# Kernel optimization log

Measured on AMD Instinct MI355X. Metric: run time of the kernel, lower is better.

Reference implementation:

```python
import jax, jax.numpy as jnp
import numpy as np
from jax import lax

B, T, I, H, C = 64, 512, 512, 1024, 1000


def _lstm_layer(x, W_ih, W_hh, b_ih, b_hh):
    # x: [B, T, in]; W_ih: [4H, in]; W_hh: [4H, H]; biases: [4H]
    # Precompute input projections for all timesteps (one big GEMM).
    xW = jnp.einsum('bti,gi->btg', x, W_ih) + b_ih + b_hh  # [B, T, 4H]
    h0 = jnp.zeros((x.shape[0], W_hh.shape[1]), x.dtype)
    c0 = jnp.zeros_like(h0)

    def step(carry, xw_t):
        h, c = carry
        gates = xw_t + h @ W_hh.T  # [B, 4H]
        i, f, g, o = jnp.split(gates, 4, axis=-1)  # PyTorch gate order i,f,g,o
        i = jax.nn.sigmoid(i)
        f = jax.nn.sigmoid(f)
        g = jnp.tanh(g)
        o = jax.nn.sigmoid(o)
        c = f * c + i * g
        h = o * jnp.tanh(c)
        return (h, c), h

    (h_T, c_T), hs = lax.scan(step, (h0, c0), jnp.swapaxes(xW, 0, 1))
    return jnp.swapaxes(hs, 0, 1), h_T  # [B, T, H], [B, H]


def setup_inputs() -> dict:
    key = jax.random.key(0)
    ks = jax.random.split(key, 11)
    s_i = 1.0 / np.sqrt(H)
    u = lambda k, shape: jax.random.uniform(k, shape, jnp.float32, -s_i, s_i)
    return {
        'x': jax.random.normal(ks[0], (B, T, I), jnp.float32),
        'W_ih0': u(ks[1], (4 * H, I)),
        'W_hh0': u(ks[2], (4 * H, H)),
        'b_ih0': u(ks[3], (4 * H,)),
        'b_hh0': u(ks[4], (4 * H,)),
        'W_ih1': u(ks[5], (4 * H, H)),
        'W_hh1': u(ks[6], (4 * H, H)),
        'b_ih1': u(ks[7], (4 * H,)),
        'b_hh1': u(ks[8], (4 * H,)),
        'W_d': u(ks[9], (C, H)),
        'b_d': u(ks[10], (C,)),
    }


def reference(x, W_ih0, W_hh0, b_ih0, b_hh0, W_ih1, W_hh1, b_ih1, b_hh1, W_d, b_d):
    h1_seq, _ = _lstm_layer(x, W_ih0, W_hh0, b_ih0, b_hh0)
    _, h_last = _lstm_layer(h1_seq, W_ih1, W_hh1, b_ih1, b_hh1)
    return h_last @ W_d.T + b_d  # [B, num_classes]
```

## Files before the change

kernel.cpp:

```cpp
#include <hip/hip_runtime.h>

typedef short short8 __attribute__((ext_vector_type(8)));
typedef float f32x4 __attribute__((ext_vector_type(4)));
typedef float f32x16 __attribute__((ext_vector_type(16)));
typedef int i32x4 __attribute__((ext_vector_type(4)));
typedef unsigned short u16;
typedef unsigned long long u64;

#define NBLK 256
#define BDIM 512
#define BB 64
#define TT 512
#define II 512
#define HH 1024
#define NCLS 1000
#define HBUF (BB*HH)

__device__ __forceinline__ u16 f2bf(float f) {
  union { float f; unsigned u; } v; v.f = f;
  unsigned u = v.u;
  u += 0x7fffu + ((u >> 16) & 1u);
  return (u16)(u >> 16);
}

__device__ __forceinline__ short8 cvt8(f32x4 a, f32x4 b) {
  short8 v;
  v[0] = (short)f2bf(a[0]); v[1] = (short)f2bf(a[1]);
  v[2] = (short)f2bf(a[2]); v[3] = (short)f2bf(a[3]);
  v[4] = (short)f2bf(b[0]); v[5] = (short)f2bf(b[1]);
  v[6] = (short)f2bf(b[2]); v[7] = (short)f2bf(b[3]);
  return v;
}

__device__ __forceinline__ unsigned ld_rlx(const unsigned* p) {
  return __hip_atomic_load(p, __ATOMIC_RELAXED, __HIP_MEMORY_SCOPE_AGENT);
}
__device__ __forceinline__ void st_rlx(unsigned* p, unsigned v) {
  __hip_atomic_store(p, v, __ATOMIC_RELAXED, __HIP_MEMORY_SCOPE_AGENT);
}

__global__ void cvt_x(const float* __restrict__ x, u16* __restrict__ xb, int n8) {
  int i = blockIdx.x * blockDim.x + threadIdx.x;
  const int stride = gridDim.x * blockDim.x;
  for (; i < n8; i += stride) {
    f32x4 a = ((const f32x4*)x)[2 * i];
    f32x4 b = ((const f32x4*)x)[2 * i + 1];
    ((short8*)xb)[i] = cvt8(a, b);
  }
}


template<int N, int B0, int MH>
__device__ __forceinline__ void run_coh(const u16* lanep,
                                        const short8 (&breg)[MH], f32x16& acc) {
  static_assert(N % 8 == 0, "");
#pragma unroll
  for (int c = 0; c < N; c += 8) {
    i32x4 av[8];
#pragma unroll
    for (int i = 0; i < 8; ++i) {
      const u16* p = lanep + (c + i) * 16;
      asm volatile("global_load_dwordx4 %0, %1, off sc0 sc1"
                   : "=v"(av[i]) : "v"(p));
    }
    asm volatile("s_waitcnt vmcnt(0)" ::: "memory");
    __builtin_amdgcn_sched_barrier(0);
#pragma unroll
    for (int i = 0; i < 8; ++i) {
      union { i32x4 q; short8 s; } u; u.q = av[i];
      acc = __builtin_amdgcn_mfma_f32_32x32x16_bf16(u.s, breg[B0 + c + i], acc, 0, 0, 0);
    }
  }
}

template<int N, int B0, int MH>
__device__ __forceinline__ void run_pb(const u16* lanep,
                                       const short8 (&breg)[MH], f32x16& acc) {
#pragma unroll
  for (int i = 0; i < N; ++i) {
    short8 av = *(const short8*)(lanep + i * 16);
    acc = __builtin_amdgcn_mfma_f32_32x32x16_bf16(av, breg[B0 + i], acc, 0, 0, 0);
  }
}

template<int N, int B0, int MH>
__device__ __forceinline__ void run_pf(const float* lanep,
                                       const short8 (&breg)[MH], f32x16& acc) {
#pragma unroll
  for (int i = 0; i < N; ++i) {
    short8 av = cvt8(*(const f32x4*)(lanep + i * 16),
                     *(const f32x4*)(lanep + i * 16 + 4));
    acc = __builtin_amdgcn_mfma_f32_32x32x16_bf16(av, breg[B0 + i], acc, 0, 0, 0);
  }
}

template<bool XBF>
__global__ __launch_bounds__(BDIM, 2) void lstm2_fused(
    const float* __restrict__ x, const u16* __restrict__ xb,
    const float* __restrict__ Wih0, const float* __restrict__ Whh0,
    const float* __restrict__ bih0, const float* __restrict__ bhh0,
    const float* __restrict__ Wih1, const float* __restrict__ Whh1,
    const float* __restrict__ bih1, const float* __restrict__ bhh1,
    u16* __restrict__ ring,
    u16* __restrict__ h1buf,
    float* __restrict__ h1f,
    unsigned* __restrict__ bar)
{
  __shared__ u16 wlds[32 * 2048];
  __shared__ float blds[32];
  float (*g4)[64][32] = (float(*)[64][32])((char*)wlds + 98304);

  const bool isL1 = (blockIdx.x >= 128);
  const int wgl = isL1 ? (int)blockIdx.x - 128 : (int)blockIdx.x;
  const int j0 = wgl * 8;
  const int KX = isL1 ? HH : II;
  const int RL = KX + HH;
  const int ROWB = RL * 2;
  const float* Wih = isL1 ? Wih1 : Wih0;
  const float* Whh = isL1 ? Whh1 : Whh0;

  {
    const int cpr = RL / 8;
    for (int idx = threadIdx.x; idx < 32 * cpr; idx += BDIM) {
      int n = idx / cpr, cb = idx - n * cpr;
      int r = ((n >> 3) << 10) + j0 + (n & 7);
      int k = cb * 8;
      const float* src = (k < KX) ? (Wih + (size_t)r * KX + k)
                                  : (Whh + (size_t)r * HH + (k - KX));
      f32x4 a = *(const f32x4*)src;
      f32x4 b = *(const f32x4*)(src + 4);
      short8 v = cvt8(a, b);
      unsigned byte = (unsigned)(n * ROWB + k * 2) ^ ((unsigned)(n & 7) << 4);
      *(short8*)((char*)wlds + byte) = v;
    }
    if (threadIdx.x < 32) {
      int n = threadIdx.x;
      int r = ((n >> 3) << 10) + j0 + (n & 7);
      blds[n] = (isL1 ? bih1[r] : bih0[r]) + (isL1 ? bhh1[r] : bhh0[r]);
    }
  }
  __syncthreads();

  const int lane = threadIdx.x & 63;
  const int wid = threadIdx.x >> 6;
  const int mp = wid & 1, kq = wid >> 1;
  const int row_a = mp * 32 + (lane & 31);
  const int sub8 = (lane >> 5) << 3;
  const char* wch = (const char*)wlds;

  const int tb = threadIdx.x >> 3, tj = threadIdx.x & 7;

  unsigned* const arrA = bar;
  unsigned* const relA = bar + 64;
  unsigned* const arrB = bar + 256;
  unsigned* const relB = bar + 320;

  float c_state = 0.f;

  auto step_tail = [&](const f32x16& acc, u16* hout, bool wf) {
    const int col = lane & 31;
    const int rbase = mp * 32 + ((lane >> 5) << 2);
#pragma unroll
    for (int r = 0; r < 16; ++r) {
      int brow = rbase + (r & 3) + ((r >> 2) << 3);
      g4[kq][brow][col] = acc[r];
    }
    __syncthreads();
    float gv[4];
#pragma unroll
    for (int g = 0; g < 4; ++g)
      gv[g] = g4[0][tb][g * 8 + tj] + g4[1][tb][g * 8 + tj]
            + g4[2][tb][g * 8 + tj] + g4[3][tb][g * 8 + tj] + blds[g * 8 + tj];
    float gi = 1.f / (1.f + __expf(-gv[0]));
    float gf = 1.f / (1.f + __expf(-gv[1]));
    float e2 = __expf(2.f * fminf(15.f, fmaxf(-15.f, gv[2])));
    float gg = (e2 - 1.f) / (e2 + 1.f);
    float go = 1.f / (1.f + __expf(-gv[3]));
    c_state = gf * c_state + gi * gg;
    float e2c = __expf(2.f * fminf(15.f, fmaxf(-15.f, c_state)));
    float th = (e2c - 1.f) / (e2c + 1.f);
    float hval = go * th;
    unsigned hu = (unsigned)f2bf(hval);
    unsigned nbv = (unsigned)__shfl_xor((int)hu, 1);
    if ((tj & 1) == 0) {
      unsigned packed = hu | (nbv << 16);
      unsigned* dst = (unsigned*)(hout + (size_t)tb * HH + j0 + tj);
      st_rlx(dst, packed);
    }
    if (wf) h1f[(size_t)tb * HH + j0 + tj] = hval;
  };

  if (!isL1) {
    short8 breg[24];
#pragma unroll
    for (int i = 0; i < 24; ++i) {
      int k = (kq * 24 + i) * 16 + sub8;
      unsigned byte = ((unsigned)((lane & 31) * ROWB + k * 2))
                      ^ ((unsigned)(lane & 7) << 4);
      breg[i] = *(const short8*)(wch + byte);
    }
    __syncthreads();

    for (int t = 0; t < TT; ++t) {
      if (t >= 3) {
        if (threadIdx.x == 0)
          while (ld_rlx(relB) < (unsigned)(t - 2)) __builtin_amdgcn_s_sleep(2);
        __syncthreads();
      }
      f32x16 acc = {};
      const u16* hb = ring + (size_t)((t + 2) % 3) * HBUF + (size_t)row_a * HH;
      if (XBF) {
        const u16* xl = xb + (size_t)t * II + (size_t)row_a * ((size_t)TT * II)
                        + kq * 384 + sub8;
        if (kq == 0)      run_pb<24, 0>(xl, breg, acc);
        else if (kq == 1) { run_pb<8, 0>(xl, breg, acc);
                            run_coh<16, 8>(hb + 0 + sub8, breg, acc); }
        else if (kq == 2) run_coh<24, 0>(hb + 256 + sub8, breg, acc);
        else              run_coh<24, 0>(hb + 640 + sub8, breg, acc);
      } else {
        const float* xl = x + (size_t)t * II + (size_t)row_a * ((size_t)TT * II)
                          + kq * 384 + sub8;
        if (kq == 0)      run_pf<24, 0>(xl, breg, acc);
        else if (kq == 1) { run_pf<8, 0>(xl, breg, acc);
                            run_coh<16, 8>(hb + 0 + sub8, breg, acc); }
        else if (kq == 2) run_coh<24, 0>(hb + 256 + sub8, breg, acc);
        else              run_coh<24, 0>(hb + 640 + sub8, breg, acc);
      }
      step_tail(acc, ring + (size_t)(t % 3) * HBUF, false);
      __syncthreads();
      if (threadIdx.x == 0) {
        unsigned old = atomicAdd(arrA, 1u);
        if (old == (unsigned)(128 * (t + 1) - 1)) st_rlx(relA, (unsigned)(t + 1));
        else if (t < TT - 1)
          while (ld_rlx(relA) < (unsigned)(t + 1)) __builtin_amdgcn_s_sleep(2);
      }
      __syncthreads();
    }
  } else {
    short8 breg[32];
#pragma unroll
    for (int i = 0; i < 32; ++i) {
      int k = (kq * 32 + i) * 16 + sub8;
      unsigned byte = ((unsigned)((lane & 31) * ROWB + k * 2))
                      ^ ((unsigned)(lane & 7) << 4);
      breg[i] = *(const short8*)(wch + byte);
    }
    __syncthreads();

    for (int t = 0; t < TT; ++t) {
      if (threadIdx.x == 0)
        while (ld_rlx(relA) < (unsigned)(t + 1)) __builtin_amdgcn_s_sleep(2);
      __syncthreads();
      f32x16 acc = {};
      const u16* lp;
      if (kq < 2)
        lp = ring + (size_t)(t % 3) * HBUF + (size_t)row_a * HH + kq * 512 + sub8;
      else
        lp = h1buf + (size_t)((t + 1) & 1) * HBUF + (size_t)row_a * HH
             + (kq - 2) * 512 + sub8;
      run_coh<32, 0>(lp, breg, acc);
      step_tail(acc, h1buf + (size_t)(t & 1) * HBUF, t == TT - 1);
      if (t < TT - 1) {
        __syncthreads();
        if (threadIdx.x == 0) {
          unsigned old = atomicAdd(arrB, 1u);
          if (old == (unsigned)(128 * (t + 1) - 1)) st_rlx(relB, (unsigned)(t + 1));
          else
            while (ld_rlx(relB) < (unsigned)(t + 1)) __builtin_amdgcn_s_sleep(2);
        }
        __syncthreads();
      }
    }
  }
}

__global__ void dense_out(const float* __restrict__ h1, const float* __restrict__ Wd,
                          const float* __restrict__ bd, float* __restrict__ out)
{
  const int b  = threadIdx.x & 63;
  const int cl = threadIdx.x >> 6;
  const int cc = blockIdx.x * 4 + cl;
  float acc = 0.f;
  const float* hrow = h1 + (size_t)b * HH;
  const float* wrow = Wd + (size_t)cc * HH;
#pragma unroll 8
  for (int k = 0; k < HH; k += 4) {
    f32x4 hv = *(const f32x4*)(hrow + k);
    f32x4 wv = *(const f32x4*)(wrow + k);
    acc += hv[0] * wv[0] + hv[1] * wv[1] + hv[2] * wv[2] + hv[3] * wv[3];
  }
  out[(size_t)b * NCLS + cc] = acc + bd[cc];
}

extern "C" void kernel_launch(void* const* d_in, const int* in_sizes, int n_in,
                              void* d_out, int out_size, void* d_ws, size_t ws_size,
                              hipStream_t stream)
{
  (void)in_sizes; (void)n_in; (void)out_size;
  const float* x    = (const float*)d_in[0];
  const float* Wih0 = (const float*)d_in[1];
  const float* Whh0 = (const float*)d_in[2];
  const float* bih0 = (const float*)d_in[3];
  const float* bhh0 = (const float*)d_in[4];
  const float* Wih1 = (const float*)d_in[5];
  const float* Whh1 = (const float*)d_in[6];
  const float* bih1 = (const float*)d_in[7];
  const float* bhh1 = (const float*)d_in[8];
  const float* Wd   = (const float*)d_in[9];
  const float* bd   = (const float*)d_in[10];

  unsigned* bar = (unsigned*)d_ws;
  float* h1f  = (float*)((char*)d_ws + 4096);
  u16* h1buf  = (u16*)((char*)d_ws + 272 * 1024);
  u16* ring   = (u16*)((char*)d_ws + 528 * 1024);
  u16* xb     = (u16*)((char*)d_ws + (1u << 20));

  const size_t needA = (1u << 20) + (size_t)BB * TT * II * 2;
  const bool tierA = (ws_size >= needA);

  hipMemsetAsync(d_ws, 0, 912 * 1024, stream);

  if (tierA) {
    hipLaunchKernelGGL(cvt_x, dim3(2048), dim3(256), 0, stream,
                       x, xb, (int)((size_t)BB * TT * II / 8));
    hipLaunchKernelGGL((lstm2_fused<true>), dim3(NBLK), dim3(BDIM), 0, stream,
                       x, xb, Wih0, Whh0, bih0, bhh0, Wih1, Whh1, bih1, bhh1,
                       ring, h1buf, h1f, bar);
  } else {
    hipLaunchKernelGGL((lstm2_fused<false>), dim3(NBLK), dim3(BDIM), 0, stream,
                       x, xb, Wih0, Whh0, bih0, bhh0, Wih1, Whh1, bih1, bhh1,
                       ring, h1buf, h1f, bar);
  }
  hipLaunchKernelGGL(dense_out, dim3(250), dim3(256), 0, stream, h1f, Wd, bd,
                     (float*)d_out);
}
```

Measured before the change: 5.521 ms.

## Replace block-level grid barriers with per-wave dependency waits and double-buffered coherent loads

The grid-wide spin barriers, where thread 0 waits and then __syncthreads, are replaced by arrive-only counters. Each wave now spins on the specific release flag its loads depend on, so waves that only read x, or that read data from an earlier step, can start without waiting for the whole grid. The ring-reuse wait for layer 0 moves to just before the h store. Separately, run_coh now uses two register buffers with partial vmcnt waits so global loads overlap MFMA work. This adds more spinning waves polling atomics and more register pressure, and the memory-ordering reasoning becomes more delicate.

```diff
diff --git a/kernel.cpp b/kernel.cpp
--- a/kernel.cpp
+++ b/kernel.cpp
@@ -38,6 +38,9 @@
 __device__ __forceinline__ void st_rlx(unsigned* p, unsigned v) {
   __hip_atomic_store(p, v, __ATOMIC_RELAXED, __HIP_MEMORY_SCOPE_AGENT);
 }
+__device__ __forceinline__ void wave_wait_ge(const unsigned* p, unsigned tgt) {
+  while (ld_rlx(p) < tgt) __builtin_amdgcn_s_sleep(1);
+}
 
 __global__ void cvt_x(const float* __restrict__ x, u16* __restrict__ xb, int n8) {
   int i = blockIdx.x * blockDim.x + threadIdx.x;
@@ -49,27 +52,42 @@
   }
 }
 
+#define ISSUE8(arr, OFF)                                                     \
+  _Pragma("unroll") for (int i_ = 0; i_ < 8; ++i_)                           \
+    asm volatile("global_load_dwordx4 %0, %1, off sc0 sc1"                   \
+                 : "=v"(arr[i_]) : "v"(lanep + ((OFF) + i_) * 16));
+#define MFMA8(arr, OFF)                                                      \
+  _Pragma("unroll") for (int i_ = 0; i_ < 8; ++i_) {                         \
+    union { i32x4 q; short8 s; } u_; u_.q = arr[i_];                         \
+    acc = __builtin_amdgcn_mfma_f32_32x32x16_bf16(u_.s, breg[B0 + (OFF) + i_],\
+                                                  acc, 0, 0, 0); }
+#define VMWAIT0 asm volatile("s_waitcnt vmcnt(0)" ::: "memory")
+#define VMWAIT8 asm volatile("s_waitcnt vmcnt(8)" ::: "memory")
+#define SCHEDB  __builtin_amdgcn_sched_barrier(0)
 
 template<int N, int B0, int MH>
 __device__ __forceinline__ void run_coh(const u16* lanep,
                                         const short8 (&breg)[MH], f32x16& acc) {
-  static_assert(N % 8 == 0, "");
-#pragma unroll
-  for (int c = 0; c < N; c += 8) {
-    i32x4 av[8];
-#pragma unroll
-    for (int i = 0; i < 8; ++i) {
-      const u16* p = lanep + (c + i) * 16;
-      asm volatile("global_load_dwordx4 %0, %1, off sc0 sc1"
-                   : "=v"(av[i]) : "v"(p));
-    }
-    asm volatile("s_waitcnt vmcnt(0)" ::: "memory");
-    __builtin_amdgcn_sched_barrier(0);
-#pragma unroll
-    for (int i = 0; i < 8; ++i) {
-      union { i32x4 q; short8 s; } u; u.q = av[i];
-      acc = __builtin_amdgcn_mfma_f32_32x32x16_bf16(u.s, breg[B0 + c + i], acc, 0, 0, 0);
-    }
+  static_assert(N == 8 || N == 16 || N == 24 || N == 32, "");
+  i32x4 avA[8], avB[8];
+  if constexpr (N == 8) {
+    ISSUE8(avA, 0);
+    VMWAIT0; SCHEDB; MFMA8(avA, 0);
+  } else if constexpr (N == 16) {
+    ISSUE8(avA, 0); ISSUE8(avB, 8);
+    VMWAIT8; SCHEDB; MFMA8(avA, 0);
+    VMWAIT0; SCHEDB; MFMA8(avB, 8);
+  } else if constexpr (N == 24) {
+    ISSUE8(avA, 0); ISSUE8(avB, 8);
+    VMWAIT8; SCHEDB; MFMA8(avA, 0); ISSUE8(avA, 16);
+    VMWAIT8; SCHEDB; MFMA8(avB, 8);
+    VMWAIT0; SCHEDB; MFMA8(avA, 16);
+  } else {
+    ISSUE8(avA, 0); ISSUE8(avB, 8);
+    VMWAIT8; SCHEDB; MFMA8(avA, 0); ISSUE8(avA, 16);
+    VMWAIT8; SCHEDB; MFMA8(avB, 8); ISSUE8(avB, 24);
+    VMWAIT8; SCHEDB; MFMA8(avA, 16);
+    VMWAIT0; SCHEDB; MFMA8(avB, 24);
   }
 }
 
@@ -157,7 +175,8 @@
 
   float c_state = 0.f;
 
-  auto step_tail = [&](const f32x16& acc, u16* hout, bool wf) {
+  auto step_tail = [&](const f32x16& acc, u16* hout, unsigned ringtgt, bool wf,
+                       unsigned* arr, unsigned* rel, int t) {
     const int col = lane & 31;
     const int rbase = mp * 32 + ((lane >> 5) << 2);
 #pragma unroll
@@ -180,6 +199,7 @@
     float e2c = __expf(2.f * fminf(15.f, fmaxf(-15.f, c_state)));
     float th = (e2c - 1.f) / (e2c + 1.f);
     float hval = go * th;
+    if (ringtgt) wave_wait_ge(relB, ringtgt);
     unsigned hu = (unsigned)f2bf(hval);
     unsigned nbv = (unsigned)__shfl_xor((int)hu, 1);
     if ((tj & 1) == 0) {
@@ -188,6 +208,11 @@
       st_rlx(dst, packed);
     }
     if (wf) h1f[(size_t)tb * HH + j0 + tj] = hval;
+    __syncthreads();
+    if (threadIdx.x == 0) {
+      unsigned old = atomicAdd(arr, 1u);
+      if (old == (unsigned)(128 * (t + 1) - 1)) st_rlx(rel, (unsigned)(t + 1));
+    }
   };
 
   if (!isL1) {
@@ -202,11 +227,6 @@
     __syncthreads();
 
     for (int t = 0; t < TT; ++t) {
-      if (t >= 3) {
-        if (threadIdx.x == 0)
-          while (ld_rlx(relB) < (unsigned)(t - 2)) __builtin_amdgcn_s_sleep(2);
-        __syncthreads();
-      }
       f32x16 acc = {};
       const u16* hb = ring + (size_t)((t + 2) % 3) * HBUF + (size_t)row_a * HH;
       if (XBF) {
@@ -214,27 +234,26 @@
                         + kq * 384 + sub8;
         if (kq == 0)      run_pb<24, 0>(xl, breg, acc);
         else if (kq == 1) { run_pb<8, 0>(xl, breg, acc);
+                            wave_wait_ge(relA, (unsigned)t);
                             run_coh<16, 8>(hb + 0 + sub8, breg, acc); }
-        else if (kq == 2) run_coh<24, 0>(hb + 256 + sub8, breg, acc);
-        else              run_coh<24, 0>(hb + 640 + sub8, breg, acc);
+        else if (kq == 2) { wave_wait_ge(relA, (unsigned)t);
+                            run_coh<24, 0>(hb + 256 + sub8, breg, acc); }
+        else              { wave_wait_ge(relA, (unsigned)t);
+                            run_coh<24, 0>(hb + 640 + sub8, breg, acc); }
       } else {
         const float* xl = x + (size_t)t * II + (size_t)row_a * ((size_t)TT * II)
                           + kq * 384 + sub8;
         if (kq == 0)      run_pf<24, 0>(xl, breg, acc);
         else if (kq == 1) { run_pf<8, 0>(xl, breg, acc);
+                            wave_wait_ge(relA, (unsigned)t);
                             run_coh<16, 8>(hb + 0 + sub8, breg, acc); }
-        else if (kq == 2) run_coh<24, 0>(hb + 256 + sub8, breg, acc);
-        else              run_coh<24, 0>(hb + 640 + sub8, breg, acc);
+        else if (kq == 2) { wave_wait_ge(relA, (unsigned)t);
+                            run_coh<24, 0>(hb + 256 + sub8, breg, acc); }
+        else              { wave_wait_ge(relA, (unsigned)t);
+                            run_coh<24, 0>(hb + 640 + sub8, breg, acc); }
       }
-      step_tail(acc, ring + (size_t)(t % 3) * HBUF, false);
-      __syncthreads();
-      if (threadIdx.x == 0) {
-        unsigned old = atomicAdd(arrA, 1u);
-        if (old == (unsigned)(128 * (t + 1) - 1)) st_rlx(relA, (unsigned)(t + 1));
-        else if (t < TT - 1)
-          while (ld_rlx(relA) < (unsigned)(t + 1)) __builtin_amdgcn_s_sleep(2);
-      }
-      __syncthreads();
+      step_tail(acc, ring + (size_t)(t % 3) * HBUF,
+                (t >= 3) ? (unsigned)(t - 2) : 0u, false, arrA, relA, t);
     }
   } else {
     short8 breg[32];
@@ -248,28 +267,20 @@
     __syncthreads();
 
     for (int t = 0; t < TT; ++t) {
-      if (threadIdx.x == 0)
-        while (ld_rlx(relA) < (unsigned)(t + 1)) __builtin_amdgcn_s_sleep(2);
-      __syncthreads();
       f32x16 acc = {};
-      const u16* lp;
-      if (kq < 2)
-        lp = ring + (size_t)(t % 3) * HBUF + (size_t)row_a * HH + kq * 512 + sub8;
-      else
-        lp = h1buf + (size_t)((t + 1) & 1) * HBUF + (size_t)row_a * HH
-             + (kq - 2) * 512 + sub8;
-      run_coh<32, 0>(lp, breg, acc);
-      step_tail(acc, h1buf + (size_t)(t & 1) * HBUF, t == TT - 1);
-      if (t < TT - 1) {
-        __syncthreads();
-        if (threadIdx.x == 0) {
-          unsigned old = atomicAdd(arrB, 1u);
-          if (old == (unsigned)(128 * (t + 1) - 1)) st_rlx(relB, (unsigned)(t + 1));
-          else
-            while (ld_rlx(relB) < (unsigned)(t + 1)) __builtin_amdgcn_s_sleep(2);
-        }
-        __syncthreads();
+      if (kq < 2) {
+        wave_wait_ge(relA, (unsigned)(t + 1));
+        const u16* lp = ring + (size_t)(t % 3) * HBUF + (size_t)row_a * HH
+                        + kq * 512 + sub8;
+        run_coh<32, 0>(lp, breg, acc);
+      } else {
+        wave_wait_ge(relB, (unsigned)t);
+        const u16* lp = h1buf + (size_t)((t + 1) & 1) * HBUF
+                        + (size_t)row_a * HH + (kq - 2) * 512 + sub8;
+        run_coh<32, 0>(lp, breg, acc);
       }
+      step_tail(acc, h1buf + (size_t)(t & 1) * HBUF, 0u, t == TT - 1,
+                arrB, relB, t);
     }
   }
 }
```

After: 4.866 ms. 1.13x faster.
